# Performance work log

Measured on AMD Instinct MI355X. Metric: run time of the kernel, lower is better.

## Reference

```python
import jax, jax.numpy as jnp
import numpy as np

LN_EPS = 1e-5  # torch LayerNorm default

def _lnorm(x):
    # LayerNorm over last dim, no affine params
    mu = jnp.mean(x, axis=-1, keepdims=True)
    var = jnp.var(x, axis=-1, keepdims=True)
    return (x - mu) / jnp.sqrt(var + LN_EPS)

def setup_inputs() -> dict:
    key = jax.random.key(0)
    k0, k1, k2, k3 = jax.random.split(key, 4)
    B, S, D, H = 4, 4096, 1024, 64
    xs_q = jax.random.normal(k0, (B, S, D), dtype=jnp.float32)
    # torch Linear(D, H, bias=False) stores weight [H, D]; we store [D, H] = W.T
    sc = 1.0 / np.sqrt(D)
    Wq = jax.random.normal(k1, (D, H), dtype=jnp.float32) * sc
    Wk = jax.random.normal(k2, (D, H), dtype=jnp.float32) * sc
    Wv = jax.random.normal(k3, (D, H), dtype=jnp.float32) * sc
    return {"xs_q": xs_q, "Wq": Wq, "Wk": Wk, "Wv": Wv}

def reference(xs_q, Wq, Wk, Wv):
    # self-attention: xs_k_v = xs_q
    qs = _lnorm(jnp.einsum('bsd,dh->bsh', xs_q, Wq))  # [B,S,H]
    ks = _lnorm(jnp.einsum('bsd,dh->bsh', xs_q, Wk))
    vs = jnp.einsum('bsd,dh->bsh', xs_q, Wv)
    scaling = 1.0 / jnp.sqrt(jnp.asarray(qs.shape[-1], dtype=qs.dtype))
    att = jnp.einsum('bqh,bkh->bqk', qs, ks)          # [B,S,S] full attention matrix
    probs = jax.nn.softmax(scaling * att, axis=-1)
    vsp = jnp.einsum('bqk,bkh->bqh', probs, vs)       # [B,S,H]
    return vsp
```

## Files before the change

### kernel.cpp

```cpp
#include <hip/hip_runtime.h>
#include <hip/hip_bf16.h>


typedef __bf16 bf16x8 __attribute__((ext_vector_type(8)));
typedef __bf16 bf16x4 __attribute__((ext_vector_type(4)));
typedef float f32x4 __attribute__((ext_vector_type(4)));

#define NROW 16384
#define DD   1024
#define HH   64
#define SS   4096
#define LS   68

static __device__ inline unsigned short f2bf_u(float x) {
  __bf16 b = (__bf16)x;
  return __builtin_bit_cast(unsigned short, b);
}
static __device__ inline uint2 pk4(float a, float b, float c, float d) {
  return make_uint2((unsigned)f2bf_u(a) | ((unsigned)f2bf_u(b) << 16),
                    (unsigned)f2bf_u(c) | ((unsigned)f2bf_u(d) << 16));
}
static __device__ inline bf16x8 ld8(const __bf16* p) {
  bf16x4 lo = *reinterpret_cast<const bf16x4*>(p);
  bf16x4 hi = *reinterpret_cast<const bf16x4*>(p + 4);
  return __builtin_shufflevector(lo, hi, 0, 1, 2, 3, 4, 5, 6, 7);
}

__global__ __launch_bounds__(256) void k_transpose_w(
    const float* __restrict__ Wq, const float* __restrict__ Wk,
    const float* __restrict__ Wv, __bf16* __restrict__ WT) {
  int idx = blockIdx.x * 256 + threadIdx.x;
  int mat = idx >> 16;
  int rem = idx & 65535;
  int k = rem >> 6, h = rem & 63;
  const float* W = (mat == 0) ? Wq : ((mat == 1) ? Wk : Wv);
  WT[(size_t)(mat * 64 + h) * DD + k] = (__bf16)W[rem];
}

__global__ __launch_bounds__(128, 2) void k_proj(
    const float* __restrict__ X, const __bf16* __restrict__ WT,
    __bf16* __restrict__ qb, __bf16* __restrict__ kbp, __bf16* __restrict__ vT) {
  __shared__ __bf16 Xs[32 * LS];
  __shared__ __bf16 Ws[192 * LS];
  const int t = threadIdx.x;
  const int lane = t & 63, w = t >> 6;
  const int quad = lane >> 4, m = lane & 15;
  const int Mb = blockIdx.x * 32;

  const int xrow = t >> 2, xk0 = (t & 3) * 8;

  f32x4 acc[12];
#pragma unroll
  for (int i = 0; i < 12; i++) acc[i] = (f32x4){0.f, 0.f, 0.f, 0.f};

  float4 xa, xb;
  bf16x8 wch[6];
  xa = *reinterpret_cast<const float4*>(&X[(size_t)(Mb + xrow) * DD + xk0]);
  xb = *reinterpret_cast<const float4*>(&X[(size_t)(Mb + xrow) * DD + xk0 + 4]);
#pragma unroll
  for (int i = 0; i < 6; i++) {
    int c = t + i * 128, wr = c >> 2, wk = (c & 3) * 8;
    wch[i] = *reinterpret_cast<const bf16x8*>(&WT[(size_t)wr * DD + wk]);
  }

  for (int ko = 0; ko < DD; ko += 32) {
    __syncthreads();
    {
      __bf16* xd = &Xs[xrow * LS + xk0];
      *reinterpret_cast<uint2*>(xd) = pk4(xa.x, xa.y, xa.z, xa.w);
      *reinterpret_cast<uint2*>(xd + 4) = pk4(xb.x, xb.y, xb.z, xb.w);
#pragma unroll
      for (int i = 0; i < 6; i++) {
        int c = t + i * 128, wr = c >> 2, wk = (c & 3) * 8;
        __bf16* wd = &Ws[wr * LS + wk];
        uint4 raw = __builtin_bit_cast(uint4, wch[i]);
        *reinterpret_cast<uint2*>(wd) = make_uint2(raw.x, raw.y);
        *reinterpret_cast<uint2*>(wd + 4) = make_uint2(raw.z, raw.w);
      }
    }
    __syncthreads();
    if (ko + 32 < DD) {
      xa = *reinterpret_cast<const float4*>(
          &X[(size_t)(Mb + xrow) * DD + ko + 32 + xk0]);
      xb = *reinterpret_cast<const float4*>(
          &X[(size_t)(Mb + xrow) * DD + ko + 32 + xk0 + 4]);
#pragma unroll
      for (int i = 0; i < 6; i++) {
        int c = t + i * 128, wr = c >> 2, wk = (c & 3) * 8;
        wch[i] = *reinterpret_cast<const bf16x8*>(
            &WT[(size_t)wr * DD + ko + 32 + wk]);
      }
    }
    bf16x8 a = ld8(&Xs[(m + 16 * w) * LS + quad * 8]);
#pragma unroll
    for (int nt = 0; nt < 12; nt++) {
      bf16x8 bfr = ld8(&Ws[(m + 16 * nt) * LS + quad * 8]);
      acc[nt] = __builtin_amdgcn_mfma_f32_16x16x32_bf16(a, bfr, acc[nt], 0, 0, 0);
    }
  }

#pragma unroll
  for (int mat = 0; mat < 2; mat++) {
#pragma unroll
    for (int reg = 0; reg < 4; reg++) {
      float s = 0.f, s2 = 0.f;
#pragma unroll
      for (int ntl = 0; ntl < 4; ntl++) {
        float x = acc[mat * 4 + ntl][reg];
        s += x; s2 += x * x;
      }
#pragma unroll
      for (int off = 1; off < 16; off <<= 1) {
        s += __shfl_xor(s, off, 64);
        s2 += __shfl_xor(s2, off, 64);
      }
      float mu = s * (1.0f / 64.0f);
      float var = s2 * (1.0f / 64.0f) - mu * mu;
      float rstd = rsqrtf(var + 1e-5f);
      float scl = (mat == 0) ? 0.125f * rstd : rstd;
#pragma unroll
      for (int ntl = 0; ntl < 4; ntl++)
        acc[mat * 4 + ntl][reg] = (acc[mat * 4 + ntl][reg] - mu) * scl;
    }
  }

  const int rowbase = Mb + 16 * w + quad * 4;
#pragma unroll
  for (int nt = 0; nt < 4; nt++)
#pragma unroll
    for (int reg = 0; reg < 4; reg++) {
      qb[(size_t)(rowbase + reg) * HH + m + 16 * nt] = (__bf16)acc[nt][reg];
      kbp[(size_t)(rowbase + reg) * HH + m + 16 * nt] = (__bf16)acc[4 + nt][reg];
    }
  const int b = Mb >> 12;
  const int s0 = (Mb & 4095) + 16 * w + quad * 4;
#pragma unroll
  for (int nt = 0; nt < 4; nt++) {
    ushort4 pk = make_ushort4(f2bf_u(acc[8 + nt][0]), f2bf_u(acc[8 + nt][1]),
                              f2bf_u(acc[8 + nt][2]), f2bf_u(acc[8 + nt][3]));
    *reinterpret_cast<ushort4*>(
        &vT[((size_t)(b * 64) + m + 16 * nt) * SS + s0]) = pk;
  }
}

__global__ __launch_bounds__(256, 4) void k_attn(
    const __bf16* __restrict__ qb, const __bf16* __restrict__ kbp,
    const __bf16* __restrict__ vT, float* __restrict__ Op,
    float* __restrict__ lp) {
  __shared__ __bf16 Klds[64 * LS];
  __shared__ __bf16 Vlds[64 * LS];
  __shared__ __bf16 Plds[4][16 * LS];
  const int t = threadIdx.x, lane = t & 63, w = t >> 6;
  const int quad = lane >> 4, m = lane & 15;
  const int qt = blockIdx.x >> 2, sp = blockIdx.x & 3;
  const int Mb = qt * 64;
  const int b = Mb >> 12;
  const size_t kvbase = (size_t)b * SS * HH;

  bf16x8 qf[2];
  {
    const int row = Mb + 16 * w + m;
    qf[0] = *reinterpret_cast<const bf16x8*>(&qb[(size_t)row * HH + quad * 8]);
    qf[1] = *reinterpret_cast<const bf16x8*>(&qb[(size_t)row * HH + 32 + quad * 8]);
  }
  bf16x8 ones;
#pragma unroll
  for (int i = 0; i < 8; i++) ones[i] = (__bf16)1.0f;

  f32x4 O[4], lac;
#pragma unroll
  for (int i = 0; i < 4; i++) O[i] = (f32x4){0.f, 0.f, 0.f, 0.f};
  lac = (f32x4){0.f, 0.f, 0.f, 0.f};

  for (int kb0 = sp * (SS / 4); kb0 < (sp + 1) * (SS / 4); kb0 += 64) {
#pragma unroll
    for (int i = 0; i < 2; i++) {
      int c = t + i * 256;
      int row = c >> 3, k0 = (c & 7) * 8;
      uint4 kd = *reinterpret_cast<const uint4*>(
          &kbp[kvbase + (size_t)(kb0 + row) * HH + k0]);
      uint4 vd = *reinterpret_cast<const uint4*>(
          &vT[(size_t)(b * 64 + row) * SS + kb0 + k0]);
      __bf16* kp = &Klds[row * LS + k0];
      __bf16* vp = &Vlds[row * LS + k0];
      *reinterpret_cast<uint2*>(kp) = make_uint2(kd.x, kd.y);
      *reinterpret_cast<uint2*>(kp + 4) = make_uint2(kd.z, kd.w);
      *reinterpret_cast<uint2*>(vp) = make_uint2(vd.x, vd.y);
      *reinterpret_cast<uint2*>(vp + 4) = make_uint2(vd.z, vd.w);
    }
    __syncthreads();

    f32x4 sc[4];
#pragma unroll
    for (int nt = 0; nt < 4; nt++) sc[nt] = (f32x4){0.f, 0.f, 0.f, 0.f};
#pragma unroll
    for (int kk = 0; kk < 2; kk++)
#pragma unroll
      for (int nt = 0; nt < 4; nt++) {
        bf16x8 bf = ld8(&Klds[(m + 16 * nt) * LS + 32 * kk + quad * 8]);
        sc[nt] = __builtin_amdgcn_mfma_f32_16x16x32_bf16(qf[kk], bf, sc[nt], 0, 0, 0);
      }

    __bf16* Pw = Plds[w];
#pragma unroll
    for (int nt = 0; nt < 4; nt++)
#pragma unroll
      for (int reg = 0; reg < 4; reg++)
        Pw[(quad * 4 + reg) * LS + m + 16 * nt] = (__bf16)__expf(sc[nt][reg]);

#pragma unroll
    for (int kk = 0; kk < 2; kk++) {
      bf16x8 pf = ld8(&Pw[m * LS + 32 * kk + quad * 8]);
      lac = __builtin_amdgcn_mfma_f32_16x16x32_bf16(ones, pf, lac, 0, 0, 0);
#pragma unroll
      for (int ht = 0; ht < 4; ht++) {
        bf16x8 vf = ld8(&Vlds[(m + 16 * ht) * LS + 32 * kk + quad * 8]);
        O[ht] = __builtin_amdgcn_mfma_f32_16x16x32_bf16(vf, pf, O[ht], 0, 0, 0);
      }
    }
    __syncthreads();
  }

  const int rowg = Mb + 16 * w + m;
  float4* obase = reinterpret_cast<float4*>(
      &Op[((size_t)sp * NROW + rowg) * HH + quad * 16]);
#pragma unroll
  for (int ht = 0; ht < 4; ht++)
    obase[ht] = make_float4(O[ht][0], O[ht][1], O[ht][2], O[ht][3]);
  if (quad == 0) lp[sp * NROW + rowg] = lac[0];
}

__global__ __launch_bounds__(256) void k_comb(const float* __restrict__ Op,
                                              const float* __restrict__ lp,
                                              float* __restrict__ out) {
  int idx = blockIdx.x * 256 + threadIdx.x;
  int row = idx >> 6, h = idx & 63;
  int soff = ((h >> 2) & 3) * 16 + (h >> 4) * 4 + (h & 3);
  size_t sbase = (size_t)row * HH + soff;
  float o = 0.f, l = 0.f;
#pragma unroll
  for (int j = 0; j < 4; j++) {
    o += Op[(size_t)j * NROW * HH + sbase];
    l += lp[j * NROW + row];
  }
  out[idx] = o / l;
}

extern "C" void kernel_launch(void* const* d_in, const int* in_sizes, int n_in,
                              void* d_out, int out_size, void* d_ws, size_t ws_size,
                              hipStream_t stream) {
  const float* X  = (const float*)d_in[0];
  const float* Wq = (const float*)d_in[1];
  const float* Wk = (const float*)d_in[2];
  const float* Wv = (const float*)d_in[3];
  float* out = (float*)d_out;
  char* ws = (char*)d_ws;

  __bf16* WT  = (__bf16*)(ws);
  __bf16* qb  = (__bf16*)(ws + (size_t)512 * 1024);
  __bf16* kbp = (__bf16*)(ws + (size_t)2560 * 1024);
  __bf16* vT  = (__bf16*)(ws + (size_t)4608 * 1024);
  float*  Op  = (float*)(ws + (size_t)6656 * 1024);
  float*  lp  = (float*)(ws + (size_t)23040 * 1024);

  hipLaunchKernelGGL(k_transpose_w, dim3(768), dim3(256), 0, stream, Wq, Wk, Wv, WT);
  hipLaunchKernelGGL(k_proj, dim3(NROW / 32), dim3(128), 0, stream, X, WT, qb, kbp, vT);
  hipLaunchKernelGGL(k_attn, dim3((NROW / 64) * 4), dim3(256), 0, stream, qb, kbp, vT, Op, lp);
  hipLaunchKernelGGL(k_comb, dim3(NROW * HH / 256), dim3(256), 0, stream, Op, lp, out);
}
```

Measured before the change: 173.0 us.

## Drop LDS staging in projection, prefetch K/V, use exp2, adaptive split-K

The projection kernel no longer stages tiles in shared memory: each lane loads its X and W fragments straight from global memory into registers and double-buffers them across the K loop, which removes the barriers. The attention kernel register-prefetches the next K/V tile while the current one is computed. It also folds log2(e) into the Q scaling so exp2f replaces __expf, raises the occupancy hint to 6, and switches to 8 key splits when the workspace is large enough. The trade-offs are redundant W reads across waves, higher register pressure, and more partial outputs for the combine pass to read.

```diff
diff --git a/kernel.cpp b/kernel.cpp
--- a/kernel.cpp
+++ b/kernel.cpp
@@ -15,10 +15,6 @@
 static __device__ inline unsigned short f2bf_u(float x) {
   __bf16 b = (__bf16)x;
   return __builtin_bit_cast(unsigned short, b);
-}
-static __device__ inline uint2 pk4(float a, float b, float c, float d) {
-  return make_uint2((unsigned)f2bf_u(a) | ((unsigned)f2bf_u(b) << 16),
-                    (unsigned)f2bf_u(c) | ((unsigned)f2bf_u(d) << 16));
 }
 static __device__ inline bf16x8 ld8(const __bf16* p) {
   bf16x4 lo = *reinterpret_cast<const bf16x4*>(p);
@@ -40,63 +36,44 @@
 __global__ __launch_bounds__(128, 2) void k_proj(
     const float* __restrict__ X, const __bf16* __restrict__ WT,
     __bf16* __restrict__ qb, __bf16* __restrict__ kbp, __bf16* __restrict__ vT) {
-  __shared__ __bf16 Xs[32 * LS];
-  __shared__ __bf16 Ws[192 * LS];
-  const int t = threadIdx.x;
-  const int lane = t & 63, w = t >> 6;
+  const int t = threadIdx.x, lane = t & 63, w = t >> 6;
   const int quad = lane >> 4, m = lane & 15;
   const int Mb = blockIdx.x * 32;
-
-  const int xrow = t >> 2, xk0 = (t & 3) * 8;
+  const int row = Mb + 16 * w + m;
+  const float* xp = &X[(size_t)row * DD + quad * 8];
+  const __bf16* wp = &WT[(size_t)m * DD + quad * 8];
 
   f32x4 acc[12];
 #pragma unroll
   for (int i = 0; i < 12; i++) acc[i] = (f32x4){0.f, 0.f, 0.f, 0.f};
 
-  float4 xa, xb;
-  bf16x8 wch[6];
-  xa = *reinterpret_cast<const float4*>(&X[(size_t)(Mb + xrow) * DD + xk0]);
-  xb = *reinterpret_cast<const float4*>(&X[(size_t)(Mb + xrow) * DD + xk0 + 4]);
-#pragma unroll
-  for (int i = 0; i < 6; i++) {
-    int c = t + i * 128, wr = c >> 2, wk = (c & 3) * 8;
-    wch[i] = *reinterpret_cast<const bf16x8*>(&WT[(size_t)wr * DD + wk]);
-  }
+  float4 xa = *reinterpret_cast<const float4*>(xp);
+  float4 xb = *reinterpret_cast<const float4*>(xp + 4);
+  bf16x8 wn[12];
+#pragma unroll
+  for (int nt = 0; nt < 12; nt++)
+    wn[nt] = *reinterpret_cast<const bf16x8*>(wp + (size_t)nt * 16 * DD);
 
   for (int ko = 0; ko < DD; ko += 32) {
-    __syncthreads();
-    {
-      __bf16* xd = &Xs[xrow * LS + xk0];
-      *reinterpret_cast<uint2*>(xd) = pk4(xa.x, xa.y, xa.z, xa.w);
-      *reinterpret_cast<uint2*>(xd + 4) = pk4(xb.x, xb.y, xb.z, xb.w);
-#pragma unroll
-      for (int i = 0; i < 6; i++) {
-        int c = t + i * 128, wr = c >> 2, wk = (c & 3) * 8;
-        __bf16* wd = &Ws[wr * LS + wk];
-        uint4 raw = __builtin_bit_cast(uint4, wch[i]);
-        *reinterpret_cast<uint2*>(wd) = make_uint2(raw.x, raw.y);
-        *reinterpret_cast<uint2*>(wd + 4) = make_uint2(raw.z, raw.w);
-      }
-    }
-    __syncthreads();
+    bf16x8 a;
+    a[0] = (__bf16)xa.x; a[1] = (__bf16)xa.y;
+    a[2] = (__bf16)xa.z; a[3] = (__bf16)xa.w;
+    a[4] = (__bf16)xb.x; a[5] = (__bf16)xb.y;
+    a[6] = (__bf16)xb.z; a[7] = (__bf16)xb.w;
+    bf16x8 wc[12];
+#pragma unroll
+    for (int nt = 0; nt < 12; nt++) wc[nt] = wn[nt];
     if (ko + 32 < DD) {
-      xa = *reinterpret_cast<const float4*>(
-          &X[(size_t)(Mb + xrow) * DD + ko + 32 + xk0]);
-      xb = *reinterpret_cast<const float4*>(
-          &X[(size_t)(Mb + xrow) * DD + ko + 32 + xk0 + 4]);
-#pragma unroll
-      for (int i = 0; i < 6; i++) {
-        int c = t + i * 128, wr = c >> 2, wk = (c & 3) * 8;
-        wch[i] = *reinterpret_cast<const bf16x8*>(
-            &WT[(size_t)wr * DD + ko + 32 + wk]);
-      }
-    }
-    bf16x8 a = ld8(&Xs[(m + 16 * w) * LS + quad * 8]);
-#pragma unroll
-    for (int nt = 0; nt < 12; nt++) {
-      bf16x8 bfr = ld8(&Ws[(m + 16 * nt) * LS + quad * 8]);
-      acc[nt] = __builtin_amdgcn_mfma_f32_16x16x32_bf16(a, bfr, acc[nt], 0, 0, 0);
-    }
+      xa = *reinterpret_cast<const float4*>(xp + ko + 32);
+      xb = *reinterpret_cast<const float4*>(xp + ko + 36);
+#pragma unroll
+      for (int nt = 0; nt < 12; nt++)
+        wn[nt] = *reinterpret_cast<const bf16x8*>(
+            wp + (size_t)nt * 16 * DD + ko + 32);
+    }
+#pragma unroll
+    for (int nt = 0; nt < 12; nt++)
+      acc[nt] = __builtin_amdgcn_mfma_f32_16x16x32_bf16(a, wc[nt], acc[nt], 0, 0, 0);
   }
 
 #pragma unroll
@@ -117,7 +94,7 @@
       float mu = s * (1.0f / 64.0f);
       float var = s2 * (1.0f / 64.0f) - mu * mu;
       float rstd = rsqrtf(var + 1e-5f);
-      float scl = (mat == 0) ? 0.125f * rstd : rstd;
+      float scl = (mat == 0) ? 0.125f * 1.44269504f * rstd : rstd;
 #pragma unroll
       for (int ntl = 0; ntl < 4; ntl++)
         acc[mat * 4 + ntl][reg] = (acc[mat * 4 + ntl][reg] - mu) * scl;
@@ -143,16 +120,18 @@
   }
 }
 
-__global__ __launch_bounds__(256, 4) void k_attn(
+__global__ __launch_bounds__(256, 6) void k_attn(
     const __bf16* __restrict__ qb, const __bf16* __restrict__ kbp,
     const __bf16* __restrict__ vT, float* __restrict__ Op,
-    float* __restrict__ lp) {
+    float* __restrict__ lp, int spbits) {
   __shared__ __bf16 Klds[64 * LS];
   __shared__ __bf16 Vlds[64 * LS];
   __shared__ __bf16 Plds[4][16 * LS];
   const int t = threadIdx.x, lane = t & 63, w = t >> 6;
   const int quad = lane >> 4, m = lane & 15;
-  const int qt = blockIdx.x >> 2, sp = blockIdx.x & 3;
+  const int nsp = 1 << spbits;
+  const int qt = blockIdx.x >> spbits, sp = blockIdx.x & (nsp - 1);
+  const int KPS = SS >> spbits;
   const int Mb = qt * 64;
   const int b = Mb >> 12;
   const size_t kvbase = (size_t)b * SS * HH;
@@ -172,23 +151,40 @@
   for (int i = 0; i < 4; i++) O[i] = (f32x4){0.f, 0.f, 0.f, 0.f};
   lac = (f32x4){0.f, 0.f, 0.f, 0.f};
 
-  for (int kb0 = sp * (SS / 4); kb0 < (sp + 1) * (SS / 4); kb0 += 64) {
-#pragma unroll
-    for (int i = 0; i < 2; i++) {
-      int c = t + i * 256;
-      int row = c >> 3, k0 = (c & 7) * 8;
-      uint4 kd = *reinterpret_cast<const uint4*>(
-          &kbp[kvbase + (size_t)(kb0 + row) * HH + k0]);
-      uint4 vd = *reinterpret_cast<const uint4*>(
-          &vT[(size_t)(b * 64 + row) * SS + kb0 + k0]);
-      __bf16* kp = &Klds[row * LS + k0];
-      __bf16* vp = &Vlds[row * LS + k0];
-      *reinterpret_cast<uint2*>(kp) = make_uint2(kd.x, kd.y);
-      *reinterpret_cast<uint2*>(kp + 4) = make_uint2(kd.z, kd.w);
-      *reinterpret_cast<uint2*>(vp) = make_uint2(vd.x, vd.y);
-      *reinterpret_cast<uint2*>(vp + 4) = make_uint2(vd.z, vd.w);
+  const int c0row = t >> 3, ck0 = (t & 7) * 8;
+  const int c1row = c0row + 32;
+  const int kb_lo = sp * KPS, kb_hi = kb_lo + KPS;
+
+  uint4 kd0, kd1, vd0, vd1;
+  {
+    kd0 = *reinterpret_cast<const uint4*>(&kbp[kvbase + (size_t)(kb_lo + c0row) * HH + ck0]);
+    kd1 = *reinterpret_cast<const uint4*>(&kbp[kvbase + (size_t)(kb_lo + c1row) * HH + ck0]);
+    vd0 = *reinterpret_cast<const uint4*>(&vT[(size_t)(b * 64 + c0row) * SS + kb_lo + ck0]);
+    vd1 = *reinterpret_cast<const uint4*>(&vT[(size_t)(b * 64 + c1row) * SS + kb_lo + ck0]);
+  }
+
+  for (int kb0 = kb_lo; kb0 < kb_hi; kb0 += 64) {
+    {
+      __bf16* kp0 = &Klds[c0row * LS + ck0];
+      __bf16* kp1 = &Klds[c1row * LS + ck0];
+      __bf16* vp0 = &Vlds[c0row * LS + ck0];
+      __bf16* vp1 = &Vlds[c1row * LS + ck0];
+      *reinterpret_cast<uint2*>(kp0) = make_uint2(kd0.x, kd0.y);
+      *reinterpret_cast<uint2*>(kp0 + 4) = make_uint2(kd0.z, kd0.w);
+      *reinterpret_cast<uint2*>(kp1) = make_uint2(kd1.x, kd1.y);
+      *reinterpret_cast<uint2*>(kp1 + 4) = make_uint2(kd1.z, kd1.w);
+      *reinterpret_cast<uint2*>(vp0) = make_uint2(vd0.x, vd0.y);
+      *reinterpret_cast<uint2*>(vp0 + 4) = make_uint2(vd0.z, vd0.w);
+      *reinterpret_cast<uint2*>(vp1) = make_uint2(vd1.x, vd1.y);
+      *reinterpret_cast<uint2*>(vp1 + 4) = make_uint2(vd1.z, vd1.w);
     }
     __syncthreads();
+    if (kb0 + 64 < kb_hi) {
+      kd0 = *reinterpret_cast<const uint4*>(&kbp[kvbase + (size_t)(kb0 + 64 + c0row) * HH + ck0]);
+      kd1 = *reinterpret_cast<const uint4*>(&kbp[kvbase + (size_t)(kb0 + 64 + c1row) * HH + ck0]);
+      vd0 = *reinterpret_cast<const uint4*>(&vT[(size_t)(b * 64 + c0row) * SS + kb0 + 64 + ck0]);
+      vd1 = *reinterpret_cast<const uint4*>(&vT[(size_t)(b * 64 + c1row) * SS + kb0 + 64 + ck0]);
+    }
 
     f32x4 sc[4];
 #pragma unroll
@@ -206,7 +202,7 @@
     for (int nt = 0; nt < 4; nt++)
 #pragma unroll
       for (int reg = 0; reg < 4; reg++)
-        Pw[(quad * 4 + reg) * LS + m + 16 * nt] = (__bf16)__expf(sc[nt][reg]);
+        Pw[(quad * 4 + reg) * LS + m + 16 * nt] = (__bf16)exp2f(sc[nt][reg]);
 
 #pragma unroll
     for (int kk = 0; kk < 2; kk++) {
@@ -232,14 +228,13 @@
 
 __global__ __launch_bounds__(256) void k_comb(const float* __restrict__ Op,
                                               const float* __restrict__ lp,
-                                              float* __restrict__ out) {
+                                              float* __restrict__ out, int nsp) {
   int idx = blockIdx.x * 256 + threadIdx.x;
   int row = idx >> 6, h = idx & 63;
   int soff = ((h >> 2) & 3) * 16 + (h >> 4) * 4 + (h & 3);
   size_t sbase = (size_t)row * HH + soff;
   float o = 0.f, l = 0.f;
-#pragma unroll
-  for (int j = 0; j < 4; j++) {
+  for (int j = 0; j < nsp; j++) {
     o += Op[(size_t)j * NROW * HH + sbase];
     l += lp[j * NROW + row];
   }
@@ -261,10 +256,15 @@
   __bf16* kbp = (__bf16*)(ws + (size_t)2560 * 1024);
   __bf16* vT  = (__bf16*)(ws + (size_t)4608 * 1024);
   float*  Op  = (float*)(ws + (size_t)6656 * 1024);
-  float*  lp  = (float*)(ws + (size_t)23040 * 1024);
+  const size_t need8 = (size_t)(6656 + 8 * 4096 + 512) * 1024;
+  const int spbits = (ws_size >= need8) ? 3 : 2;
+  const int nsp = 1 << spbits;
+  float* lp = (float*)(ws + (size_t)(6656 + nsp * 4096) * 1024);
 
   hipLaunchKernelGGL(k_transpose_w, dim3(768), dim3(256), 0, stream, Wq, Wk, Wv, WT);
   hipLaunchKernelGGL(k_proj, dim3(NROW / 32), dim3(128), 0, stream, X, WT, qb, kbp, vT);
-  hipLaunchKernelGGL(k_attn, dim3((NROW / 64) * 4), dim3(256), 0, stream, qb, kbp, vT, Op, lp);
-  hipLaunchKernelGGL(k_comb, dim3(NROW * HH / 256), dim3(256), 0, stream, Op, lp, out);
-}
+  hipLaunchKernelGGL(k_attn, dim3((NROW / 64) * nsp), dim3(256), 0, stream,
+                     qb, kbp, vT, Op, lp, spbits);
+  hipLaunchKernelGGL(k_comb, dim3(NROW * HH / 256), dim3(256), 0, stream,
+                     Op, lp, out, nsp);
+}
```

Result: slower. 197.3 us (+14.0%).
